# Optimization experiments

Hardware: AMD Instinct MI355X
Metric: run time of the kernel (lower is better)

Reference implementation:

```python
import jax, jax.numpy as jnp
import numpy as np

NEG_SLOPE = 0.2  # DGL GATConv default negative_slope


def gat_conv(x, W, attn_l, attn_r, bias, src, dst, n_nodes):
    """DGL-style GATConv. x:[N,F_in], W:[F_in,H*D], attn_l/attn_r/bias:[H,D].
    Returns [N,H,D]."""
    H, D = attn_l.shape
    feat = (x @ W).reshape(n_nodes, H, D)            # projected features
    el = jnp.sum(feat * attn_l, axis=-1)              # [N,H]
    er = jnp.sum(feat * attn_r, axis=-1)              # [N,H]
    e = jax.nn.leaky_relu(el[src] + er[dst], NEG_SLOPE)  # [E,H] per-edge score
    # edge softmax over incoming edges of each dst node (numerically stable)
    m = jax.ops.segment_max(e, dst, num_segments=n_nodes)   # [N,H]
    a = jnp.exp(e - m[dst])
    denom = jax.ops.segment_sum(a, dst, num_segments=n_nodes)
    alpha = a / denom[dst]                            # [E,H]
    msg = feat[src] * alpha[..., None]                # [E,H,D]
    out = jax.ops.segment_sum(msg, dst, num_segments=n_nodes)  # [N,H,D]
    return out + bias


def setup_inputs() -> dict:
    key = jax.random.key(0)
    ks = jax.random.split(key, 12)
    N, E = 50000, 800000
    F_in, D1, H1, F_out = 128, 32, 4, 64
    h = jax.random.normal(ks[0], (N, F_in), dtype=jnp.float32)
    src = jax.random.randint(ks[1], (E,), 0, N, dtype=jnp.int32)
    dst = jax.random.randint(ks[2], (E,), 0, N, dtype=jnp.int32)
    s1 = 1.0 / np.sqrt(F_in)
    s2 = 1.0 / np.sqrt(H1 * D1)
    W1 = jax.random.normal(ks[3], (F_in, H1 * D1), dtype=jnp.float32) * s1
    al1 = jax.random.normal(ks[4], (H1, D1), dtype=jnp.float32) * s1
    ar1 = jax.random.normal(ks[5], (H1, D1), dtype=jnp.float32) * s1
    b1 = jnp.zeros((H1, D1), dtype=jnp.float32)
    W2 = jax.random.normal(ks[6], (H1 * D1, 1 * F_out), dtype=jnp.float32) * s2
    al2 = jax.random.normal(ks[7], (1, F_out), dtype=jnp.float32) * s2
    ar2 = jax.random.normal(ks[8], (1, F_out), dtype=jnp.float32) * s2
    b2 = jnp.zeros((1, F_out), dtype=jnp.float32)
    return {"h": h, "src": src, "dst": dst,
            "W1": W1, "al1": al1, "ar1": ar1, "b1": b1,
            "W2": W2, "al2": al2, "ar2": ar2, "b2": b2}


def reference(h, src, dst, W1, al1, ar1, b1, W2, al2, ar2, b2):
    N = h.shape[0]
    x = gat_conv(h, W1, al1, ar1, b1, src, dst, N)   # [N,H,D]
    x = jax.nn.relu(x.reshape(N, -1))                # flatten heads + ReLU
    # dropout(p=0.2) is identity in eval mode
    x = gat_conv(x, W2, al2, ar2, b2, src, dst, N)   # [N,1,F_out]
    return x.squeeze(1)
```

## Files before the change

kernel.cpp:

```cpp
#include <hip/hip_runtime.h>

#define NEG_SLOPE 0.2f
#define CH 4096
#define BSTRIDE 1536

__device__ inline unsigned short f2bf(float f) {
    unsigned u = __float_as_uint(f);
    unsigned r = (u + 0x7FFFu + ((u >> 16) & 1u)) >> 16;
    return (unsigned short)r;
}
__device__ inline unsigned pack2bf(float a, float b) {
    return (unsigned)f2bf(a) | ((unsigned)f2bf(b) << 16);
}
__device__ inline float bf2f_lo(unsigned u) { return __uint_as_float(u << 16); }
__device__ inline float bf2f_hi(unsigned u) { return __uint_as_float(u & 0xFFFF0000u); }
__device__ inline float lrelu(float v) { return v > 0.f ? v : NEG_SLOPE * v; }

#define FMA8(A, F, S)                          \
    A[0] = fmaf(bf2f_lo((F).x), S, A[0]);      \
    A[1] = fmaf(bf2f_hi((F).x), S, A[1]);      \
    A[2] = fmaf(bf2f_lo((F).y), S, A[2]);      \
    A[3] = fmaf(bf2f_hi((F).y), S, A[3]);      \
    A[4] = fmaf(bf2f_lo((F).z), S, A[4]);      \
    A[5] = fmaf(bf2f_hi((F).z), S, A[5]);      \
    A[6] = fmaf(bf2f_lo((F).w), S, A[6]);      \
    A[7] = fmaf(bf2f_hi((F).w), S, A[7]);

__global__ __launch_bounds__(256) void csrP_gemm1_kernel(
    const int* __restrict__ src, const int* __restrict__ dst,
    int* __restrict__ bucket_cursor, unsigned* __restrict__ tmp, int E, int NB,
    int nchunks, const float* __restrict__ h, const float* __restrict__ W1,
    const float* __restrict__ al1, const float* __restrict__ ar1,
    unsigned short* __restrict__ feat1b, float* __restrict__ el1,
    float* __restrict__ er1, int N) {
    __shared__ __align__(16) int smem[8192];
    const int tid = threadIdx.x;
    if ((int)blockIdx.x < nchunks) {
        int* lh = smem;
        int* lex = smem + 1024;
        int* gbase_sh = smem + 2048;
        int* wsum = smem + 3072;
        unsigned* sortedv = (unsigned*)(smem + 3104);
        const int base_e = blockIdx.x * CH;
        const int cnt_e = min(CH, E - base_e);
        for (int i = tid; i < 1024; i += 256) lh[i] = 0;
        __syncthreads();
        for (int i = tid; i < cnt_e; i += 256) atomicAdd(&lh[dst[base_e + i] >> 6], 1);
        __syncthreads();
        const int lane = tid & 63;
        const int wid = tid >> 6;
        int s0 = lh[tid * 4], s1 = lh[tid * 4 + 1], s2 = lh[tid * 4 + 2],
            s3 = lh[tid * 4 + 3];
        int tot = s0 + s1 + s2 + s3;
        int inc = tot;
#pragma unroll
        for (int off = 1; off < 64; off <<= 1) {
            int t = __shfl_up(inc, off, 64);
            if (lane >= off) inc += t;
        }
        if (lane == 63) wsum[wid] = inc;
        __syncthreads();
        int wbase = 0;
#pragma unroll
        for (int k = 0; k < 4; ++k)
            if (k < wid) wbase += wsum[k];
        int ebase = wbase + inc - tot;
        lex[tid * 4] = ebase;
        lex[tid * 4 + 1] = ebase + s0;
        lex[tid * 4 + 2] = ebase + s0 + s1;
        lex[tid * 4 + 3] = ebase + s0 + s1 + s2;
        for (int b = tid; b < NB; b += 256) {
            int c = lh[b];
            gbase_sh[b] = c ? atomicAdd(&bucket_cursor[b], c) : 0;
        }
        __syncthreads();
        for (int i = tid; i < 1024; i += 256) lh[i] = 0;
        __syncthreads();
        for (int i = tid; i < cnt_e; i += 256) {
            int e = base_e + i;
            int d = dst[e];
            unsigned b = (unsigned)d >> 6;
            int r = atomicAdd(&lh[b], 1);
            sortedv[lex[b] + r] =
                (b << 22) | ((unsigned)(d & 63) << 16) | (unsigned)(src[e] & 0xFFFF);
        }
        __syncthreads();
        for (int i = tid; i < cnt_e; i += 256) {
            unsigned v = sortedv[i];
            int b = v >> 22;
            int pos = gbase_sh[b] + (i - lex[b]);
            if (pos < BSTRIDE)
                tmp[(size_t)b * BSTRIDE + pos] = v;
        }
    } else {
        float* xs = (float*)smem;
        const int row0 = ((int)blockIdx.x - nchunks) * 64;
        {
            const float4* s4 = (const float4*)h;
            float4* d4 = (float4*)xs;
            int base4 = row0 * 32;
            int tot4 = N * 32;
            for (int i = tid; i < 2048; i += 256)
                if (base4 + i < tot4) d4[i] = s4[base4 + i];
        }
        __syncthreads();
        const int lane = tid & 31;
        const int c0 = lane * 4;
        const int r0 = (tid >> 5) * 8;
        float acc[8][4] = {};
#pragma unroll 2
        for (int k0 = 0; k0 < 128; k0 += 4) {
            float4 wv0 = *(const float4*)(W1 + (k0 + 0) * 128 + c0);
            float4 wv1 = *(const float4*)(W1 + (k0 + 1) * 128 + c0);
            float4 wv2 = *(const float4*)(W1 + (k0 + 2) * 128 + c0);
            float4 wv3 = *(const float4*)(W1 + (k0 + 3) * 128 + c0);
            float4 xv[8];
#pragma unroll
            for (int r = 0; r < 8; ++r)
                xv[r] = *(const float4*)(xs + (r0 + r) * 128 + k0);
#pragma unroll
            for (int r = 0; r < 8; ++r) {
                acc[r][0] = fmaf(xv[r].x, wv0.x, acc[r][0]);
                acc[r][1] = fmaf(xv[r].x, wv0.y, acc[r][1]);
                acc[r][2] = fmaf(xv[r].x, wv0.z, acc[r][2]);
                acc[r][3] = fmaf(xv[r].x, wv0.w, acc[r][3]);
                acc[r][0] = fmaf(xv[r].y, wv1.x, acc[r][0]);
                acc[r][1] = fmaf(xv[r].y, wv1.y, acc[r][1]);
                acc[r][2] = fmaf(xv[r].y, wv1.z, acc[r][2]);
                acc[r][3] = fmaf(xv[r].y, wv1.w, acc[r][3]);
                acc[r][0] = fmaf(xv[r].z, wv2.x, acc[r][0]);
                acc[r][1] = fmaf(xv[r].z, wv2.y, acc[r][1]);
                acc[r][2] = fmaf(xv[r].z, wv2.z, acc[r][2]);
                acc[r][3] = fmaf(xv[r].z, wv2.w, acc[r][3]);
                acc[r][0] = fmaf(xv[r].w, wv3.x, acc[r][0]);
                acc[r][1] = fmaf(xv[r].w, wv3.y, acc[r][1]);
                acc[r][2] = fmaf(xv[r].w, wv3.z, acc[r][2]);
                acc[r][3] = fmaf(xv[r].w, wv3.w, acc[r][3]);
            }
        }
        float4 alv = *(const float4*)(al1 + c0);
        float4 arv = *(const float4*)(ar1 + c0);
#pragma unroll
        for (int r = 0; r < 8; ++r) {
            int row = row0 + r0 + r;
            if (row < N) {
                ushort4 fb;
                fb.x = f2bf(acc[r][0]);
                fb.y = f2bf(acc[r][1]);
                fb.z = f2bf(acc[r][2]);
                fb.w = f2bf(acc[r][3]);
                *(ushort4*)(feat1b + (size_t)row * 128 + c0) = fb;
                float pl = acc[r][0] * alv.x + acc[r][1] * alv.y + acc[r][2] * alv.z +
                           acc[r][3] * alv.w;
                float pr = acc[r][0] * arv.x + acc[r][1] * arv.y + acc[r][2] * arv.z +
                           acc[r][3] * arv.w;
#pragma unroll
                for (int off = 4; off >= 1; off >>= 1) {
                    pl += __shfl_xor(pl, off, 32);
                    pr += __shfl_xor(pr, off, 32);
                }
                if ((lane & 7) == 0) {
                    el1[row * 4 + (lane >> 3)] = pl;
                    er1[row * 4 + (lane >> 3)] = pr;
                }
            }
        }
    }
}

__global__ __launch_bounds__(256) void gemm2_fused(const unsigned short* __restrict__ out1b,
                                                   const float* __restrict__ W2,
                                                   const float* __restrict__ al2,
                                                   const float* __restrict__ ar2,
                                                   unsigned short* __restrict__ feat2b,
                                                   float* __restrict__ el2,
                                                   float* __restrict__ er2, int N) {
    __shared__ float xs[64 * 128];
    const int tid = threadIdx.x;
    const int row0 = blockIdx.x * 64;
    {
        const uint4* s8 = (const uint4*)out1b;
        int base8 = row0 * 16;
        int tot8 = N * 16;
        for (int i = tid; i < 1024; i += 256)
            if (base8 + i < tot8) {
                uint4 v = s8[base8 + i];
                float* o = xs + i * 8;
                o[0] = bf2f_lo(v.x);
                o[1] = bf2f_hi(v.x);
                o[2] = bf2f_lo(v.y);
                o[3] = bf2f_hi(v.y);
                o[4] = bf2f_lo(v.z);
                o[5] = bf2f_hi(v.z);
                o[6] = bf2f_lo(v.w);
                o[7] = bf2f_hi(v.w);
            }
    }
    __syncthreads();
    const int lane = tid & 15;
    const int c0 = lane * 4;
    const int r0 = (tid >> 4) * 4;
    float acc[4][4] = {};
    for (int k0 = 0; k0 < 128; k0 += 8) {
        float4 wv[8];
#pragma unroll
        for (int kk = 0; kk < 8; ++kk)
            wv[kk] = *(const float4*)(W2 + (k0 + kk) * 64 + c0);
#pragma unroll
        for (int kk = 0; kk < 8; ++kk) {
#pragma unroll
            for (int r = 0; r < 4; ++r) {
                float x = xs[(r0 + r) * 128 + k0 + kk];
                acc[r][0] = fmaf(x, wv[kk].x, acc[r][0]);
                acc[r][1] = fmaf(x, wv[kk].y, acc[r][1]);
                acc[r][2] = fmaf(x, wv[kk].z, acc[r][2]);
                acc[r][3] = fmaf(x, wv[kk].w, acc[r][3]);
            }
        }
    }
    float4 alv = *(const float4*)(al2 + c0);
    float4 arv = *(const float4*)(ar2 + c0);
#pragma unroll
    for (int r = 0; r < 4; ++r) {
        int row = row0 + r0 + r;
        if (row < N) {
            ushort4 fb;
            fb.x = f2bf(acc[r][0]);
            fb.y = f2bf(acc[r][1]);
            fb.z = f2bf(acc[r][2]);
            fb.w = f2bf(acc[r][3]);
            *(ushort4*)(feat2b + (size_t)row * 64 + c0) = fb;
            float pl = acc[r][0] * alv.x + acc[r][1] * alv.y + acc[r][2] * alv.z +
                       acc[r][3] * alv.w;
            float pr = acc[r][0] * arv.x + acc[r][1] * arv.y + acc[r][2] * arv.z +
                       acc[r][3] * arv.w;
#pragma unroll
            for (int off = 8; off >= 1; off >>= 1) {
                pl += __shfl_xor(pl, off, 16);
                pr += __shfl_xor(pr, off, 16);
            }
            if (lane == 0) {
                el2[row] = pl;
                er2[row] = pr;
            }
        }
    }
}

__global__ __launch_bounds__(512) void gather1_kernel(const unsigned* __restrict__ tmp,
                                                      const int* __restrict__ bucket_cursor,
                                                      const float* __restrict__ el1,
                                                      const float* __restrict__ er1,
                                                      const unsigned short* __restrict__ feat1b,
                                                      const float* __restrict__ b1,
                                                      unsigned short* __restrict__ out1b,
                                                      int N) {
    __shared__ __align__(16) float a_all[4096];
    __shared__ int ssrc[BSTRIDE];
    __shared__ int dh[64], dex[64], dcur[64];
    unsigned* sval = (unsigned*)a_all;
    const int tid = threadIdx.x;
    const int b = (int)blockIdx.x >> 1;
    const int half = (int)blockIdx.x & 1;
    const int gb = b * BSTRIDE;
    const int cnt = min(bucket_cursor[b], BSTRIDE);
    if (tid < 64) dh[tid] = 0;
    __syncthreads();
    for (int i = tid; i < cnt; i += 512) {
        unsigned v = tmp[gb + i];
        sval[i] = v;
        atomicAdd(&dh[(v >> 16) & 63], 1);
    }
    __syncthreads();
    if (tid < 64) {
        int v = dh[tid], inc = v;
#pragma unroll
        for (int off = 1; off < 64; off <<= 1) {
            int t = __shfl_up(inc, off, 64);
            if (tid >= off) inc += t;
        }
        dex[tid] = inc - v;
        dcur[tid] = inc - v;
    }
    __syncthreads();
    for (int i = tid; i < cnt; i += 512) {
        unsigned val = sval[i];
        int dl = (val >> 16) & 63;
        int pos = atomicAdd(&dcur[dl], 1);
        ssrc[pos] = (int)((unsigned)(dl << 16) | (val & 0xFFFFu));
    }
    __syncthreads();
    const int begH = half ? dex[32] : 0;
    const int endH = half ? cnt : dex[32];
    for (int i = begH + tid; i < endH; i += 512) {
        int val = ssrc[i];
        int s = val & 0xFFFF;
        int dl = val >> 16;
        float4 el4 = *(const float4*)(el1 + (size_t)s * 4);
        float4 er4 = *(const float4*)(er1 + (size_t)(b * 64 + dl) * 4);
        float v0 = __expf(lrelu(el4.x + er4.x));
        float v1 = __expf(lrelu(el4.y + er4.y));
        float v2 = __expf(lrelu(el4.z + er4.z));
        float v3 = __expf(lrelu(el4.w + er4.w));
        int idx = i - begH;
        if (idx < 1024) *(float4*)&a_all[idx * 4] = make_float4(v0, v1, v2, v3);
    }
    __syncthreads();
    const int w = tid >> 6;
    const int lane = tid & 63;
    const int q = lane >> 4;
    const int l16 = lane & 15;
    const int c0 = l16 * 8;
    const int hh = l16 >> 2;
    float4 bv0 = *(const float4*)(b1 + c0);
    float4 bv1 = *(const float4*)(b1 + c0 + 4);
    for (int k = 0; k < 4; ++k) {
        const int dl = half * 32 + w * 4 + k;
        const int d = b * 64 + dl;
        if (d >= N) break;
        const int baseA = dex[dl];
        const int baseR = baseA - begH;
        const int M = dh[dl];
        float acc[8] = {}, bcc[8] = {};
        float den = 0.f;
        int e = q;
        for (; e + 12 < M; e += 16) {
            int s0 = ssrc[baseA + e] & 0xFFFF;
            int s1 = ssrc[baseA + e + 4] & 0xFFFF;
            int s2 = ssrc[baseA + e + 8] & 0xFFFF;
            int s3 = ssrc[baseA + e + 12] & 0xFFFF;
            float a0 = a_all[(baseR + e) * 4 + hh];
            float a1 = a_all[(baseR + e + 4) * 4 + hh];
            float a2 = a_all[(baseR + e + 8) * 4 + hh];
            float a3 = a_all[(baseR + e + 12) * 4 + hh];
            uint4 f0 = *(const uint4*)(feat1b + (size_t)s0 * 128 + c0);
            uint4 f1 = *(const uint4*)(feat1b + (size_t)s1 * 128 + c0);
            uint4 f2 = *(const uint4*)(feat1b + (size_t)s2 * 128 + c0);
            uint4 f3 = *(const uint4*)(feat1b + (size_t)s3 * 128 + c0);
            den += (a0 + a1) + (a2 + a3);
            FMA8(acc, f0, a0);
            FMA8(bcc, f1, a1);
            FMA8(acc, f2, a2);
            FMA8(bcc, f3, a3);
        }
        for (; e < M; e += 4) {
            int s0 = ssrc[baseA + e] & 0xFFFF;
            float a0 = a_all[(baseR + e) * 4 + hh];
            uint4 f0 = *(const uint4*)(feat1b + (size_t)s0 * 128 + c0);
            den += a0;
            FMA8(acc, f0, a0);
        }
#pragma unroll
        for (int j = 0; j < 8; ++j) {
            acc[j] += bcc[j];
            acc[j] += __shfl_xor(acc[j], 16, 64);
            acc[j] += __shfl_xor(acc[j], 32, 64);
        }
        den += __shfl_xor(den, 16, 64);
        den += __shfl_xor(den, 32, 64);
        if (q == 0) {
            float inv = (M > 0) ? 1.f / den : 0.f;
            uint4 o;
            o.x = pack2bf(fmaxf(acc[0] * inv + bv0.x, 0.f), fmaxf(acc[1] * inv + bv0.y, 0.f));
            o.y = pack2bf(fmaxf(acc[2] * inv + bv0.z, 0.f), fmaxf(acc[3] * inv + bv0.w, 0.f));
            o.z = pack2bf(fmaxf(acc[4] * inv + bv1.x, 0.f), fmaxf(acc[5] * inv + bv1.y, 0.f));
            o.w = pack2bf(fmaxf(acc[6] * inv + bv1.z, 0.f), fmaxf(acc[7] * inv + bv1.w, 0.f));
            *(uint4*)(out1b + (size_t)d * 128 + c0) = o;
        }
    }
}

__global__ __launch_bounds__(512) void gather2_kernel(const unsigned* __restrict__ tmp,
                                                      const int* __restrict__ bucket_cursor,
                                                      const float* __restrict__ el2,
                                                      const float* __restrict__ er2,
                                                      const unsigned short* __restrict__ feat2b,
                                                      const float* __restrict__ b2,
                                                      float* __restrict__ out2, int N) {
    __shared__ __align__(16) float a_all[BSTRIDE];
    __shared__ int ssrc[BSTRIDE];
    __shared__ int dh[64], dex[64], dcur[64];
    unsigned* sval = (unsigned*)a_all;
    const int tid = threadIdx.x;
    const int b = (int)blockIdx.x >> 1;
    const int half = (int)blockIdx.x & 1;
    const int gb = b * BSTRIDE;
    const int cnt = min(bucket_cursor[b], BSTRIDE);
    if (tid < 64) dh[tid] = 0;
    __syncthreads();
    for (int i = tid; i < cnt; i += 512) {
        unsigned v = tmp[gb + i];
        sval[i] = v;
        atomicAdd(&dh[(v >> 16) & 63], 1);
    }
    __syncthreads();
    if (tid < 64) {
        int v = dh[tid], inc = v;
#pragma unroll
        for (int off = 1; off < 64; off <<= 1) {
            int t = __shfl_up(inc, off, 64);
            if (tid >= off) inc += t;
        }
        dex[tid] = inc - v;
        dcur[tid] = inc - v;
    }
    __syncthreads();
    for (int i = tid; i < cnt; i += 512) {
        unsigned val = sval[i];
        int dl = (val >> 16) & 63;
        int pos = atomicAdd(&dcur[dl], 1);
        ssrc[pos] = (int)((unsigned)(dl << 16) | (val & 0xFFFFu));
    }
    __syncthreads();
    const int begH = half ? dex[32] : 0;
    const int endH = half ? cnt : dex[32];
    for (int i = begH + tid; i < endH; i += 512) {
        int val = ssrc[i];
        int s = val & 0xFFFF;
        int dl = val >> 16;
        float v = el2[s] + er2[b * 64 + dl];
        a_all[i] = __expf(lrelu(v));
    }
    __syncthreads();
    const int w = tid >> 6;
    const int lane = tid & 63;
    const int oct = lane >> 3;
    const int l8 = lane & 7;
    const int c0 = l8 * 8;
    float4 bv0 = *(const float4*)(b2 + c0);
    float4 bv1 = *(const float4*)(b2 + c0 + 4);
    for (int k = 0; k < 4; ++k) {
        const int dl = half * 32 + w * 4 + k;
        const int d = b * 64 + dl;
        if (d >= N) break;
        const int base = dex[dl];
        const int M = dh[dl];
        float acc[8] = {}, bcc[8] = {};
        float den = 0.f;
        int e = oct;
        for (; e + 8 < M; e += 16) {
            int s0 = ssrc[base + e] & 0xFFFF;
            int s1 = ssrc[base + e + 8] & 0xFFFF;
            float a0 = a_all[base + e];
            float a1 = a_all[base + e + 8];
            uint4 f0 = *(const uint4*)(feat2b + (size_t)s0 * 64 + c0);
            uint4 f1 = *(const uint4*)(feat2b + (size_t)s1 * 64 + c0);
            den += a0 + a1;
            FMA8(acc, f0, a0);
            FMA8(bcc, f1, a1);
        }
        while (e < M) {
            int s0 = ssrc[base + e] & 0xFFFF;
            float a0 = a_all[base + e];
            uint4 f0 = *(const uint4*)(feat2b + (size_t)s0 * 64 + c0);
            den += a0;
            FMA8(acc, f0, a0);
            e += 8;
        }
#pragma unroll
        for (int j = 0; j < 8; ++j) {
            acc[j] += bcc[j];
            acc[j] += __shfl_xor(acc[j], 8, 64);
            acc[j] += __shfl_xor(acc[j], 16, 64);
            acc[j] += __shfl_xor(acc[j], 32, 64);
        }
        den += __shfl_xor(den, 8, 64);
        den += __shfl_xor(den, 16, 64);
        den += __shfl_xor(den, 32, 64);
        if (oct == 0) {
            float inv = (M > 0) ? 1.f / den : 0.f;
            *(float4*)(out2 + (size_t)d * 64 + c0) =
                make_float4(acc[0] * inv + bv0.x, acc[1] * inv + bv0.y,
                            acc[2] * inv + bv0.z, acc[3] * inv + bv0.w);
            *(float4*)(out2 + (size_t)d * 64 + c0 + 4) =
                make_float4(acc[4] * inv + bv1.x, acc[5] * inv + bv1.y,
                            acc[6] * inv + bv1.z, acc[7] * inv + bv1.w);
        }
    }
}

extern "C" void kernel_launch(void* const* d_in, const int* in_sizes, int n_in,
                              void* d_out, int out_size, void* d_ws, size_t ws_size,
                              hipStream_t stream) {
    const float* h   = (const float*)d_in[0];
    const int*   src = (const int*)d_in[1];
    const int*   dst = (const int*)d_in[2];
    const float* W1  = (const float*)d_in[3];
    const float* al1 = (const float*)d_in[4];
    const float* ar1 = (const float*)d_in[5];
    const float* b1  = (const float*)d_in[6];
    const float* W2  = (const float*)d_in[7];
    const float* al2 = (const float*)d_in[8];
    const float* ar2 = (const float*)d_in[9];
    const float* b2  = (const float*)d_in[10];

    const int N = in_sizes[0] / 128;
    const int E = in_sizes[1];
    const int NB = (N + 63) >> 6;

    char* ws = (char*)d_ws;
    size_t off = 0;
    auto alloc = [&](size_t elems) -> void* {
        void* p = (void*)(ws + off);
        off += ((elems * 4 + 255) / 256) * 256;
        return p;
    };
    int* bucket_cursor = (int*)alloc(NB);
    unsigned* tmp      = (unsigned*)alloc((size_t)NB * BSTRIDE);
    float* el1   = (float*)alloc((size_t)N * 4);
    float* er1   = (float*)alloc((size_t)N * 4);
    unsigned short* feat1b = (unsigned short*)alloc((size_t)N * 64);
    unsigned short* out1b  = (unsigned short*)alloc((size_t)N * 64);
    float* el2   = (float*)alloc(N);
    float* er2   = (float*)alloc(N);
    unsigned short* feat2b = (unsigned short*)alloc((size_t)N * 32);
    float* out2  = (float*)d_out;

    const int nchunks = (E + CH - 1) / CH;
    const int gemm1_blocks = (N + 63) / 64;

    hipMemsetAsync(bucket_cursor, 0, (size_t)NB * 4, stream);
    csrP_gemm1_kernel<<<nchunks + gemm1_blocks, 256, 0, stream>>>(
        src, dst, bucket_cursor, tmp, E, NB, nchunks, h, W1, al1, ar1, feat1b,
        el1, er1, N);

    gather1_kernel<<<NB * 2, 512, 0, stream>>>(tmp, bucket_cursor, el1, er1,
                                               feat1b, b1, out1b, N);

    gemm2_fused<<<(N + 63) / 64, 256, 0, stream>>>(out1b, W2, al2, ar2, feat2b, el2,
                                                   er2, N);
    gather2_kernel<<<NB * 2, 512, 0, stream>>>(tmp, bucket_cursor, el2, er2,
                                               feat2b, b2, out2, N);
}
```

Baseline: 209.7 us.

## Fuse layer-2 projection GEMM into layer-1 gather kernel epilogue

The layer-1 aggregation now keeps its 32 bf16 output rows per block in shared memory and computes the layer-2 projection, feat2 and el2/er2 directly in the same kernel. This removes the out1b global round trip and one kernel launch. In exchange it adds shared memory use per block, which may lower occupancy in the gather, and W2 is read from global by every block without the row reuse the separate GEMM tile had.

```diff
diff --git a/kernel.cpp b/kernel.cpp
--- a/kernel.cpp
+++ b/kernel.cpp
@@ -168,96 +168,17 @@
     }
 }
 
-__global__ __launch_bounds__(256) void gemm2_fused(const unsigned short* __restrict__ out1b,
-                                                   const float* __restrict__ W2,
-                                                   const float* __restrict__ al2,
-                                                   const float* __restrict__ ar2,
-                                                   unsigned short* __restrict__ feat2b,
-                                                   float* __restrict__ el2,
-                                                   float* __restrict__ er2, int N) {
-    __shared__ float xs[64 * 128];
-    const int tid = threadIdx.x;
-    const int row0 = blockIdx.x * 64;
-    {
-        const uint4* s8 = (const uint4*)out1b;
-        int base8 = row0 * 16;
-        int tot8 = N * 16;
-        for (int i = tid; i < 1024; i += 256)
-            if (base8 + i < tot8) {
-                uint4 v = s8[base8 + i];
-                float* o = xs + i * 8;
-                o[0] = bf2f_lo(v.x);
-                o[1] = bf2f_hi(v.x);
-                o[2] = bf2f_lo(v.y);
-                o[3] = bf2f_hi(v.y);
-                o[4] = bf2f_lo(v.z);
-                o[5] = bf2f_hi(v.z);
-                o[6] = bf2f_lo(v.w);
-                o[7] = bf2f_hi(v.w);
-            }
-    }
-    __syncthreads();
-    const int lane = tid & 15;
-    const int c0 = lane * 4;
-    const int r0 = (tid >> 4) * 4;
-    float acc[4][4] = {};
-    for (int k0 = 0; k0 < 128; k0 += 8) {
-        float4 wv[8];
-#pragma unroll
-        for (int kk = 0; kk < 8; ++kk)
-            wv[kk] = *(const float4*)(W2 + (k0 + kk) * 64 + c0);
-#pragma unroll
-        for (int kk = 0; kk < 8; ++kk) {
-#pragma unroll
-            for (int r = 0; r < 4; ++r) {
-                float x = xs[(r0 + r) * 128 + k0 + kk];
-                acc[r][0] = fmaf(x, wv[kk].x, acc[r][0]);
-                acc[r][1] = fmaf(x, wv[kk].y, acc[r][1]);
-                acc[r][2] = fmaf(x, wv[kk].z, acc[r][2]);
-                acc[r][3] = fmaf(x, wv[kk].w, acc[r][3]);
-            }
-        }
-    }
-    float4 alv = *(const float4*)(al2 + c0);
-    float4 arv = *(const float4*)(ar2 + c0);
-#pragma unroll
-    for (int r = 0; r < 4; ++r) {
-        int row = row0 + r0 + r;
-        if (row < N) {
-            ushort4 fb;
-            fb.x = f2bf(acc[r][0]);
-            fb.y = f2bf(acc[r][1]);
-            fb.z = f2bf(acc[r][2]);
-            fb.w = f2bf(acc[r][3]);
-            *(ushort4*)(feat2b + (size_t)row * 64 + c0) = fb;
-            float pl = acc[r][0] * alv.x + acc[r][1] * alv.y + acc[r][2] * alv.z +
-                       acc[r][3] * alv.w;
-            float pr = acc[r][0] * arv.x + acc[r][1] * arv.y + acc[r][2] * arv.z +
-                       acc[r][3] * arv.w;
-#pragma unroll
-            for (int off = 8; off >= 1; off >>= 1) {
-                pl += __shfl_xor(pl, off, 16);
-                pr += __shfl_xor(pr, off, 16);
-            }
-            if (lane == 0) {
-                el2[row] = pl;
-                er2[row] = pr;
-            }
-        }
-    }
-}
-
-__global__ __launch_bounds__(512) void gather1_kernel(const unsigned* __restrict__ tmp,
-                                                      const int* __restrict__ bucket_cursor,
-                                                      const float* __restrict__ el1,
-                                                      const float* __restrict__ er1,
-                                                      const unsigned short* __restrict__ feat1b,
-                                                      const float* __restrict__ b1,
-                                                      unsigned short* __restrict__ out1b,
-                                                      int N) {
+__global__ __launch_bounds__(512) void gather1_gemm2_kernel(
+    const unsigned* __restrict__ tmp, const int* __restrict__ bucket_cursor,
+    const float* __restrict__ el1, const float* __restrict__ er1,
+    const unsigned short* __restrict__ feat1b, const float* __restrict__ b1,
+    const float* __restrict__ W2, const float* __restrict__ al2,
+    const float* __restrict__ ar2, unsigned short* __restrict__ feat2b,
+    float* __restrict__ el2, float* __restrict__ er2, int N) {
     __shared__ __align__(16) float a_all[4096];
     __shared__ int ssrc[BSTRIDE];
     __shared__ int dh[64], dex[64], dcur[64];
+    __shared__ __align__(16) unsigned out1s[32 * 68];
     unsigned* sval = (unsigned*)a_all;
     const int tid = threadIdx.x;
     const int b = (int)blockIdx.x >> 1;
@@ -365,7 +286,54 @@
             o.y = pack2bf(fmaxf(acc[2] * inv + bv0.z, 0.f), fmaxf(acc[3] * inv + bv0.w, 0.f));
             o.z = pack2bf(fmaxf(acc[4] * inv + bv1.x, 0.f), fmaxf(acc[5] * inv + bv1.y, 0.f));
             o.w = pack2bf(fmaxf(acc[6] * inv + bv1.z, 0.f), fmaxf(acc[7] * inv + bv1.w, 0.f));
-            *(uint4*)(out1b + (size_t)d * 128 + c0) = o;
+            const int rb = w * 4 + k;
+            *(uint4*)&out1s[rb * 68 + l16 * 4] = o;
+        }
+    }
+    __syncthreads();
+    {
+        const int l16b = tid & 15;
+        const int cc0 = l16b * 4;
+        const int r = tid >> 4;
+        const int d = b * 64 + half * 32 + r;
+        float a2[4] = {};
+        for (int k0 = 0; k0 < 128; k0 += 8) {
+            uint4 xv = *(const uint4*)&out1s[r * 68 + (k0 >> 1)];
+            const float* wp = W2 + k0 * 64 + cc0;
+            float4 wv[8];
+#pragma unroll
+            for (int kk = 0; kk < 8; ++kk)
+                wv[kk] = *(const float4*)(wp + kk * 64);
+#pragma unroll
+            for (int kk = 0; kk < 8; ++kk) {
+                unsigned uv = ((const unsigned*)&xv)[kk >> 1];
+                float x = (kk & 1) ? bf2f_hi(uv) : bf2f_lo(uv);
+                a2[0] = fmaf(x, wv[kk].x, a2[0]);
+                a2[1] = fmaf(x, wv[kk].y, a2[1]);
+                a2[2] = fmaf(x, wv[kk].z, a2[2]);
+                a2[3] = fmaf(x, wv[kk].w, a2[3]);
+            }
+        }
+        float4 alv = *(const float4*)(al2 + cc0);
+        float4 arv = *(const float4*)(ar2 + cc0);
+        float pl = a2[0] * alv.x + a2[1] * alv.y + a2[2] * alv.z + a2[3] * alv.w;
+        float pr = a2[0] * arv.x + a2[1] * arv.y + a2[2] * arv.z + a2[3] * arv.w;
+#pragma unroll
+        for (int off = 8; off >= 1; off >>= 1) {
+            pl += __shfl_xor(pl, off, 16);
+            pr += __shfl_xor(pr, off, 16);
+        }
+        if (d < N) {
+            ushort4 fb;
+            fb.x = f2bf(a2[0]);
+            fb.y = f2bf(a2[1]);
+            fb.z = f2bf(a2[2]);
+            fb.w = f2bf(a2[3]);
+            *(ushort4*)(feat2b + (size_t)d * 64 + cc0) = fb;
+            if (l16b == 0) {
+                el2[d] = pl;
+                er2[d] = pr;
+            }
         }
     }
 }
@@ -510,7 +478,6 @@
     float* el1   = (float*)alloc((size_t)N * 4);
     float* er1   = (float*)alloc((size_t)N * 4);
     unsigned short* feat1b = (unsigned short*)alloc((size_t)N * 64);
-    unsigned short* out1b  = (unsigned short*)alloc((size_t)N * 64);
     float* el2   = (float*)alloc(N);
     float* er2   = (float*)alloc(N);
     unsigned short* feat2b = (unsigned short*)alloc((size_t)N * 32);
@@ -524,11 +491,10 @@
         src, dst, bucket_cursor, tmp, E, NB, nchunks, h, W1, al1, ar1, feat1b,
         el1, er1, N);
 
-    gather1_kernel<<<NB * 2, 512, 0, stream>>>(tmp, bucket_cursor, el1, er1,
-                                               feat1b, b1, out1b, N);
-
-    gemm2_fused<<<(N + 63) / 64, 256, 0, stream>>>(out1b, W2, al2, ar2, feat2b, el2,
-                                                   er2, N);
+    gather1_gemm2_kernel<<<NB * 2, 512, 0, stream>>>(tmp, bucket_cursor, el1, er1,
+                                                     feat1b, b1, W2, al2, ar2,
+                                                     feat2b, el2, er2, N);
+
     gather2_kernel<<<NB * 2, 512, 0, stream>>>(tmp, bucket_cursor, el2, er2,
                                                feat2b, b2, out2, N);
 }
```

Result: slower. 240.4 us (+14.7%).

## Map one destination per lane group in gathers, drop cross-lane reductions

Applied to the files above, without the earlier changes.

Both gather kernels now give each 16-lane (layer 1) or 8-lane (layer 2) group its own destination node and have it walk that node's edges sequentially. Before, a whole wavefront split one node's edges and then combined the partial sums with shuffle reductions. The shuffles and the idle lanes at output time go away. gather2 now launches one block per bucket instead of two, so the bucket's sort work is not done twice. gather1's edge-score pass is reorganised per destination so the er row is loaded once per node instead of once per edge. The cost is longer serial edge loops per group, load imbalance across groups when degrees differ, and fewer blocks in gather2.

```diff
diff --git a/kernel.cpp b/kernel.cpp
--- a/kernel.cpp
+++ b/kernel.cpp
@@ -287,86 +287,88 @@
         unsigned val = sval[i];
         int dl = (val >> 16) & 63;
         int pos = atomicAdd(&dcur[dl], 1);
-        ssrc[pos] = (int)((unsigned)(dl << 16) | (val & 0xFFFFu));
+        ssrc[pos] = (int)(val & 0xFFFFu);
     }
     __syncthreads();
     const int begH = half ? dex[32] : 0;
     const int endH = half ? cnt : dex[32];
-    for (int i = begH + tid; i < endH; i += 512) {
-        int val = ssrc[i];
-        int s = val & 0xFFFF;
-        int dl = val >> 16;
-        float4 el4 = *(const float4*)(el1 + (size_t)s * 4);
-        float4 er4 = *(const float4*)(er1 + (size_t)(b * 64 + dl) * 4);
-        float v0 = __expf(lrelu(el4.x + er4.x));
-        float v1 = __expf(lrelu(el4.y + er4.y));
-        float v2 = __expf(lrelu(el4.z + er4.z));
-        float v3 = __expf(lrelu(el4.w + er4.w));
-        int idx = i - begH;
-        if (idx < 1024) *(float4*)&a_all[idx * 4] = make_float4(v0, v1, v2, v3);
+    {
+        const int w = tid >> 6;
+        const int lane = tid & 63;
+        for (int dl = half * 32 + w * 4; dl < half * 32 + w * 4 + 4; ++dl) {
+            const int base = dex[dl];
+            const int M = dh[dl];
+            float4 er4 = *(const float4*)(er1 + (size_t)(b * 64 + dl) * 4);
+            for (int i = lane; i < M; i += 64) {
+                int s = ssrc[base + i];
+                float4 el4 = *(const float4*)(el1 + (size_t)s * 4);
+                float v0 = __expf(lrelu(el4.x + er4.x));
+                float v1 = __expf(lrelu(el4.y + er4.y));
+                float v2 = __expf(lrelu(el4.z + er4.z));
+                float v3 = __expf(lrelu(el4.w + er4.w));
+                int idx = base + i - begH;
+                if (idx < 1024)
+                    *(float4*)&a_all[idx * 4] = make_float4(v0, v1, v2, v3);
+            }
+        }
     }
     __syncthreads();
     const int w = tid >> 6;
     const int lane = tid & 63;
-    const int q = lane >> 4;
+    const int g = lane >> 4;
     const int l16 = lane & 15;
     const int c0 = l16 * 8;
     const int hh = l16 >> 2;
-    float4 bv0 = *(const float4*)(b1 + c0);
-    float4 bv1 = *(const float4*)(b1 + c0 + 4);
-    for (int k = 0; k < 4; ++k) {
-        const int dl = half * 32 + w * 4 + k;
-        const int d = b * 64 + dl;
-        if (d >= N) break;
+    const int dl = half * 32 + w * 4 + g;
+    const int d = b * 64 + dl;
+    if (d < N) {
         const int baseA = dex[dl];
         const int baseR = baseA - begH;
         const int M = dh[dl];
+        float4 bv0 = *(const float4*)(b1 + c0);
+        float4 bv1 = *(const float4*)(b1 + c0 + 4);
         float acc[8] = {}, bcc[8] = {};
-        float den = 0.f;
-        int e = q;
-        for (; e + 12 < M; e += 16) {
-            int s0 = ssrc[baseA + e] & 0xFFFF;
-            int s1 = ssrc[baseA + e + 4] & 0xFFFF;
-            int s2 = ssrc[baseA + e + 8] & 0xFFFF;
-            int s3 = ssrc[baseA + e + 12] & 0xFFFF;
+        float den = 0.f, dbn = 0.f;
+        int e = 0;
+        for (; e + 3 < M; e += 4) {
+            int s0 = ssrc[baseA + e];
+            int s1 = ssrc[baseA + e + 1];
+            int s2 = ssrc[baseA + e + 2];
+            int s3 = ssrc[baseA + e + 3];
             float a0 = a_all[(baseR + e) * 4 + hh];
-            float a1 = a_all[(baseR + e + 4) * 4 + hh];
-            float a2 = a_all[(baseR + e + 8) * 4 + hh];
-            float a3 = a_all[(baseR + e + 12) * 4 + hh];
+            float a1 = a_all[(baseR + e + 1) * 4 + hh];
+            float a2 = a_all[(baseR + e + 2) * 4 + hh];
+            float a3 = a_all[(baseR + e + 3) * 4 + hh];
             uint4 f0 = *(const uint4*)(feat1b + (size_t)s0 * 128 + c0);
             uint4 f1 = *(const uint4*)(feat1b + (size_t)s1 * 128 + c0);
             uint4 f2 = *(const uint4*)(feat1b + (size_t)s2 * 128 + c0);
             uint4 f3 = *(const uint4*)(feat1b + (size_t)s3 * 128 + c0);
-            den += (a0 + a1) + (a2 + a3);
+            den += a0 + a2;
+            dbn += a1 + a3;
             FMA8(acc, f0, a0);
             FMA8(bcc, f1, a1);
             FMA8(acc, f2, a2);
             FMA8(bcc, f3, a3);
         }
-        for (; e < M; e += 4) {
-            int s0 = ssrc[baseA + e] & 0xFFFF;
+        for (; e < M; ++e) {
+            int s0 = ssrc[baseA + e];
             float a0 = a_all[(baseR + e) * 4 + hh];
             uint4 f0 = *(const uint4*)(feat1b + (size_t)s0 * 128 + c0);
             den += a0;
             FMA8(acc, f0, a0);
         }
-#pragma unroll
-        for (int j = 0; j < 8; ++j) {
-            acc[j] += bcc[j];
-            acc[j] += __shfl_xor(acc[j], 16, 64);
-            acc[j] += __shfl_xor(acc[j], 32, 64);
-        }
-        den += __shfl_xor(den, 16, 64);
-        den += __shfl_xor(den, 32, 64);
-        if (q == 0) {
-            float inv = (M > 0) ? 1.f / den : 0.f;
-            uint4 o;
-            o.x = pack2bf(fmaxf(acc[0] * inv + bv0.x, 0.f), fmaxf(acc[1] * inv + bv0.y, 0.f));
-            o.y = pack2bf(fmaxf(acc[2] * inv + bv0.z, 0.f), fmaxf(acc[3] * inv + bv0.w, 0.f));
-            o.z = pack2bf(fmaxf(acc[4] * inv + bv1.x, 0.f), fmaxf(acc[5] * inv + bv1.y, 0.f));
-            o.w = pack2bf(fmaxf(acc[6] * inv + bv1.z, 0.f), fmaxf(acc[7] * inv + bv1.w, 0.f));
-            *(uint4*)(out1b + (size_t)d * 128 + c0) = o;
-        }
+        den += dbn;
+        float inv = (M > 0) ? 1.f / den : 0.f;
+        uint4 o;
+        o.x = pack2bf(fmaxf((acc[0] + bcc[0]) * inv + bv0.x, 0.f),
+                      fmaxf((acc[1] + bcc[1]) * inv + bv0.y, 0.f));
+        o.y = pack2bf(fmaxf((acc[2] + bcc[2]) * inv + bv0.z, 0.f),
+                      fmaxf((acc[3] + bcc[3]) * inv + bv0.w, 0.f));
+        o.z = pack2bf(fmaxf((acc[4] + bcc[4]) * inv + bv1.x, 0.f),
+                      fmaxf((acc[5] + bcc[5]) * inv + bv1.y, 0.f));
+        o.w = pack2bf(fmaxf((acc[6] + bcc[6]) * inv + bv1.z, 0.f),
+                      fmaxf((acc[7] + bcc[7]) * inv + bv1.w, 0.f));
+        *(uint4*)(out1b + (size_t)d * 128 + c0) = o;
     }
 }
 
@@ -382,8 +384,7 @@
     __shared__ int dh[64], dex[64], dcur[64];
     unsigned* sval = (unsigned*)a_all;
     const int tid = threadIdx.x;
-    const int b = (int)blockIdx.x >> 1;
-    const int half = (int)blockIdx.x & 1;
+    const int b = (int)blockIdx.x;
     const int gb = b * BSTRIDE;
     const int cnt = min(bucket_cursor[b], BSTRIDE);
     if (tid < 64) dh[tid] = 0;
@@ -412,9 +413,7 @@
         ssrc[pos] = (int)((unsigned)(dl << 16) | (val & 0xFFFFu));
     }
     __syncthreads();
-    const int begH = half ? dex[32] : 0;
-    const int endH = half ? cnt : dex[32];
-    for (int i = begH + tid; i < endH; i += 512) {
+    for (int i = tid; i < cnt; i += 512) {
         int val = ssrc[i];
         int s = val & 0xFFFF;
         int dl = val >> 16;
@@ -424,58 +423,54 @@
     __syncthreads();
     const int w = tid >> 6;
     const int lane = tid & 63;
-    const int oct = lane >> 3;
+    const int g = lane >> 3;
     const int l8 = lane & 7;
     const int c0 = l8 * 8;
-    float4 bv0 = *(const float4*)(b2 + c0);
-    float4 bv1 = *(const float4*)(b2 + c0 + 4);
-    for (int k = 0; k < 4; ++k) {
-        const int dl = half * 32 + w * 4 + k;
-        const int d = b * 64 + dl;
-        if (d >= N) break;
+    const int dl = w * 8 + g;
+    const int d = b * 64 + dl;
+    if (d < N) {
         const int base = dex[dl];
         const int M = dh[dl];
+        float4 bv0 = *(const float4*)(b2 + c0);
+        float4 bv1 = *(const float4*)(b2 + c0 + 4);
         float acc[8] = {}, bcc[8] = {};
-        float den = 0.f;
-        int e = oct;
-        for (; e + 8 < M; e += 16) {
+        float den = 0.f, dbn = 0.f;
+        int e = 0;
+        for (; e + 3 < M; e += 4) {
             int s0 = ssrc[base + e] & 0xFFFF;
-            int s1 = ssrc[base + e + 8] & 0xFFFF;
+            int s1 = ssrc[base + e + 1] & 0xFFFF;
+            int s2 = ssrc[base + e + 2] & 0xFFFF;
+            int s3 = ssrc[base + e + 3] & 0xFFFF;
             float a0 = a_all[base + e];
-            float a1 = a_all[base + e + 8];
+            float a1 = a_all[base + e + 1];
+            float a2 = a_all[base + e + 2];
+            float a3 = a_all[base + e + 3];
             uint4 f0 = *(const uint4*)(feat2b + (size_t)s0 * 64 + c0);
             uint4 f1 = *(const uint4*)(feat2b + (size_t)s1 * 64 + c0);
-            den += a0 + a1;
+            uint4 f2 = *(const uint4*)(feat2b + (size_t)s2 * 64 + c0);
+            uint4 f3 = *(const uint4*)(feat2b + (size_t)s3 * 64 + c0);
+            den += a0 + a2;
+            dbn += a1 + a3;
             FMA8(acc, f0, a0);
             FMA8(bcc, f1, a1);
-        }
-        while (e < M) {
+            FMA8(acc, f2, a2);
+            FMA8(bcc, f3, a3);
+        }
+        for (; e < M; ++e) {
             int s0 = ssrc[base + e] & 0xFFFF;
             float a0 = a_all[base + e];
             uint4 f0 = *(const uint4*)(feat2b + (size_t)s0 * 64 + c0);
             den += a0;
             FMA8(acc, f0, a0);
-            e += 8;
-        }
-#pragma unroll
-        for (int j = 0; j < 8; ++j) {
-            acc[j] += bcc[j];
-            acc[j] += __shfl_xor(acc[j], 8, 64);
-            acc[j] += __shfl_xor(acc[j], 16, 64);
-            acc[j] += __shfl_xor(acc[j], 32, 64);
-        }
-        den += __shfl_xor(den, 8, 64);
-        den += __shfl_xor(den, 16, 64);
-        den += __shfl_xor(den, 32, 64);
-        if (oct == 0) {
-            float inv = (M > 0) ? 1.f / den : 0.f;
-            *(float4*)(out2 + (size_t)d * 64 + c0) =
-                make_float4(acc[0] * inv + bv0.x, acc[1] * inv + bv0.y,
-                            acc[2] * inv + bv0.z, acc[3] * inv + bv0.w);
-            *(float4*)(out2 + (size_t)d * 64 + c0 + 4) =
-                make_float4(acc[4] * inv + bv1.x, acc[5] * inv + bv1.y,
-                            acc[6] * inv + bv1.z, acc[7] * inv + bv1.w);
-        }
+        }
+        den += dbn;
+        float inv = (M > 0) ? 1.f / den : 0.f;
+        *(float4*)(out2 + (size_t)d * 64 + c0) =
+            make_float4((acc[0] + bcc[0]) * inv + bv0.x, (acc[1] + bcc[1]) * inv + bv0.y,
+                        (acc[2] + bcc[2]) * inv + bv0.z, (acc[3] + bcc[3]) * inv + bv0.w);
+        *(float4*)(out2 + (size_t)d * 64 + c0 + 4) =
+            make_float4((acc[4] + bcc[4]) * inv + bv1.x, (acc[5] + bcc[5]) * inv + bv1.y,
+                        (acc[6] + bcc[6]) * inv + bv1.z, (acc[7] + bcc[7]) * inv + bv1.w);
     }
 }
 
@@ -529,6 +524,6 @@
 
     gemm2_fused<<<(N + 63) / 64, 256, 0, stream>>>(out1b, W2, al2, ar2, feat2b, el2,
                                                    er2, N);
-    gather2_kernel<<<NB * 2, 512, 0, stream>>>(tmp, bucket_cursor, el2, er2,
-                                               feat2b, b2, out2, N);
-}
+    gather2_kernel<<<NB, 512, 0, stream>>>(tmp, bucket_cursor, el2, er2,
+                                           feat2b, b2, out2, N);
+}
```

Measured after the change: 198.7 us. 1.06x faster.
